# Kernel optimization log

Measured on AMD Instinct MI355X. Metric: run time of the kernel, lower is better.

Reference implementation:

```python
import jax, jax.numpy as jnp
import numpy as np

THRESHOLD = 0.5
NEG_POS_RATIO = 3
ALPHA = 1.0
B, P, C, O = 128, 8732, 21, 32


def xy_to_cxcy(xy):
    return jnp.concatenate([(xy[..., 2:] + xy[..., :2]) / 2, xy[..., 2:] - xy[..., :2]], axis=-1)


def cxcy_to_xy(cxcy):
    return jnp.concatenate([cxcy[..., :2] - cxcy[..., 2:] / 2, cxcy[..., :2] + cxcy[..., 2:] / 2], axis=-1)


def cxcy_to_gcxgcy(cxcy, priors_cxcy):
    g_cxcy = (cxcy[..., :2] - priors_cxcy[..., :2]) / (priors_cxcy[..., 2:] / 10.0)
    g_wh = jnp.log(cxcy[..., 2:] / priors_cxcy[..., 2:]) * 5.0
    return jnp.concatenate([g_cxcy, g_wh], axis=-1)


def find_jaccard_overlap(set1, set2):
    # set1: [O,4] xy, set2: [P,4] xy -> [O,P]
    lo = jnp.maximum(set1[:, None, :2], set2[None, :, :2])
    hi = jnp.minimum(set1[:, None, 2:], set2[None, :, 2:])
    inter = jnp.prod(jnp.clip(hi - lo, 0.0), axis=-1)
    a1 = jnp.prod(set1[:, 2:] - set1[:, :2], axis=-1)
    a2 = jnp.prod(set2[:, 2:] - set2[:, :2], axis=-1)
    union = a1[:, None] + a2[None, :] - inter
    return inter / union


def setup_inputs() -> dict:
    key = jax.random.key(0)
    k0, k1, k2, k3, k4, k5, k6 = jax.random.split(key, 7)
    predicted_locs = jax.random.normal(k0, (B, P, 4), jnp.float32)
    predicted_scores = jax.random.normal(k1, (B, P, C), jnp.float32)
    centers = jax.random.uniform(k2, (B, O, 2), jnp.float32, 0.2, 0.8)
    sizes = jax.random.uniform(k3, (B, O, 2), jnp.float32, 0.05, 0.3)
    boxes = jnp.concatenate([centers - sizes / 2, centers + sizes / 2], axis=-1)
    labels = jax.random.randint(k4, (B, O), 0, C)
    p_c = jax.random.uniform(k5, (P, 2), jnp.float32, 0.05, 0.95)
    p_wh = jax.random.uniform(k6, (P, 2), jnp.float32, 0.05, 0.5)
    priors_cxcy = jnp.concatenate([p_c, p_wh], axis=-1)
    return {"predicted_locs": predicted_locs, "predicted_scores": predicted_scores,
            "boxes": boxes, "labels": labels, "priors_cxcy": priors_cxcy}


def reference(predicted_locs, predicted_scores, boxes, labels, priors_cxcy):
    priors_xy = cxcy_to_xy(priors_cxcy)

    def match_one(boxes_i, labels_i):
        overlap = find_jaccard_overlap(boxes_i, priors_xy)           # [O,P]
        overlap_for_each_prior = jnp.max(overlap, axis=0)            # [P]
        object_for_each_prior = jnp.argmax(overlap, axis=0)          # [P]
        prior_for_each_object = jnp.argmax(overlap, axis=1)          # [O]
        object_for_each_prior = object_for_each_prior.at[prior_for_each_object].set(jnp.arange(O))
        overlap_for_each_prior = overlap_for_each_prior.at[prior_for_each_object].set(1.0)
        label_for_each_prior = labels_i[object_for_each_prior]
        label_for_each_prior = jnp.where(overlap_for_each_prior < THRESHOLD, 0, label_for_each_prior)
        true_locs_i = cxcy_to_gcxgcy(xy_to_cxcy(boxes_i[object_for_each_prior]), priors_cxcy)
        return label_for_each_prior, true_locs_i

    true_classes, true_locs = jax.vmap(match_one)(boxes, labels)     # [B,P], [B,P,4]

    positive = true_classes != 0                                     # [B,P]
    n_positives = jnp.sum(positive, axis=1)                          # [B]
    n_pos_total = jnp.sum(n_positives)

    # L1Loss (mean over selected positive elements, 4 per prior)
    abs_diff = jnp.abs(predicted_locs - true_locs)                   # [B,P,4]
    loc_loss = jnp.sum(abs_diff * positive[..., None]) / (n_pos_total.astype(jnp.float32) * 4.0)

    # per-element cross-entropy
    log_p = jax.nn.log_softmax(predicted_scores, axis=-1)            # [B,P,C]
    conf_loss_all = -jnp.take_along_axis(log_p, true_classes[..., None], axis=-1)[..., 0]  # [B,P]

    conf_loss_pos_sum = jnp.sum(jnp.where(positive, conf_loss_all, 0.0))
    conf_loss_neg = jnp.where(positive, 0.0, conf_loss_all)
    conf_loss_neg_sorted = -jnp.sort(-conf_loss_neg, axis=1)         # descending
    n_hard = NEG_POS_RATIO * n_positives                             # [B]
    hard_mask = jnp.arange(P)[None, :] < n_hard[:, None]             # [B,P]
    conf_loss_hard_neg_sum = jnp.sum(jnp.where(hard_mask, conf_loss_neg_sorted, 0.0))

    conf_loss = (conf_loss_hard_neg_sum + conf_loss_pos_sum) / n_pos_total.astype(jnp.float32)
    return conf_loss + ALPHA * loc_loss
```

## Files before the change

### kernel.cpp

```cpp
#include <hip/hip_runtime.h>
#include <hip/hip_bf16.h>

#define NB 128
#define NP 8732
#define NO 32
#define NC 21


__global__ __launch_bounds__(256) void k_init(int* ws) {
    int i = blockIdx.x * 256 + threadIdx.x;
    const int n = 36352 / 4;
    if (i < n) ws[i] = 0;
}

__global__ __launch_bounds__(256) void k_match(const float* __restrict__ boxes,
                                               const float* __restrict__ priors,
                                               int* __restrict__ code,
                                               unsigned long long* __restrict__ packed) {
    int b = blockIdx.y;
    int base = blockIdx.x * 1024 + threadIdx.x;
    int lane = threadIdx.x & 63;

    __shared__ float4 sbox[NO];
    if (threadIdx.x < NO)
        sbox[threadIdx.x] = ((const float4*)(boxes + (size_t)b * NO * 4))[threadIdx.x];
    __syncthreads();

    int   pidx[4];
    float px1[4], py1[4], px2[4], py2[4], pa[4];
    float bestv[4];
    int   besto[4];
#pragma unroll
    for (int j = 0; j < 4; ++j) {
        int p = base + 256 * j;
        pidx[j] = p;
        int pp = p < NP ? p : NP - 1;
        float4 pr = ((const float4*)priors)[pp];
        px1[j] = pr.x - pr.z * 0.5f; py1[j] = pr.y - pr.w * 0.5f;
        px2[j] = pr.x + pr.z * 0.5f; py2[j] = pr.y + pr.w * 0.5f;
        pa[j]  = (px2[j] - px1[j]) * (py2[j] - py1[j]);
        bestv[j] = -1.0f; besto[j] = 0;
    }

    for (int o = 0; o < NO; ++o) {
        float4 bx = sbox[o];
        float a1 = (bx.z - bx.x) * (bx.w - bx.y);
        unsigned long long pk = 0ull;
#pragma unroll
        for (int j = 0; j < 4; ++j) {
            float lx = fmaxf(bx.x, px1[j]), ly = fmaxf(bx.y, py1[j]);
            float hx = fminf(bx.z, px2[j]), hy = fminf(bx.w, py2[j]);
            float iw = fmaxf(hx - lx, 0.0f), ih = fmaxf(hy - ly, 0.0f);
            float inter = iw * ih;
            float iou = inter / (a1 + pa[j] - inter);
            if (iou > bestv[j]) { bestv[j] = iou; besto[j] = o; }
            if (pidx[j] < NP) {
                unsigned long long key =
                    ((unsigned long long)__float_as_uint(iou) << 32) |
                    (unsigned long long)(0xFFFFFFFFu - (unsigned)pidx[j]);
                if (key > pk) pk = key;
            }
        }
        for (int s = 32; s > 0; s >>= 1) {
            unsigned long long other = __shfl_xor(pk, s, 64);
            if (other > pk) pk = other;
        }
        if (lane == 0) atomicMax(&packed[b * NO + o], pk);
    }
#pragma unroll
    for (int j = 0; j < 4; ++j)
        if (pidx[j] < NP)
            code[(size_t)b * NP + pidx[j]] = besto[j] | (bestv[j] >= 0.5f ? 256 : 0);
}

__global__ void k_force(int* __restrict__ code,
                        const unsigned long long* __restrict__ packed) {
    int b = threadIdx.x;
    if (b >= NB) return;
    for (int o = 0; o < NO; ++o) {
        unsigned long long pk = packed[b * NO + o];
        unsigned p = 0xFFFFFFFFu - (unsigned)(pk & 0xFFFFFFFFull);
        if (p < NP) code[(size_t)b * NP + p] = o | 256;
    }
}

__global__ __launch_bounds__(256) void k_loss(const float* __restrict__ plocs,
                                              const float* __restrict__ scores,
                                              const float* __restrict__ boxes,
                                              const int* __restrict__ labels,
                                              const float* __restrict__ priors,
                                              const int* __restrict__ code,
                                              float* __restrict__ confneg,
                                              int* __restrict__ npos,
                                              double* __restrict__ accb) {
    __shared__ float srow[256 * NC];
    int b = blockIdx.y;
    int p0 = blockIdx.x * 256;
    int cnt = NP - p0; if (cnt > 256) cnt = 256;
    int nf4 = cnt * NC / 4;
    const float4* src4 = (const float4*)(scores + ((size_t)b * NP + p0) * NC);
    for (int i = threadIdx.x; i < nf4; i += 256)
        ((float4*)srow)[i] = src4[i];
    __syncthreads();

    int p = p0 + threadIdx.x;
    float posconf = 0.0f, locpart = 0.0f;
    int isp = 0;

    if (p < NP) {
        int cd = code[(size_t)b * NP + p];
        int obj = cd & 255;
        int lbl = (cd & 256) ? labels[b * NO + obj] : 0;

        const float* s = srow + threadIdx.x * NC;
        float m = s[0];
#pragma unroll
        for (int c = 1; c < NC; ++c) m = fmaxf(m, s[c]);
        float sum = 0.0f;
#pragma unroll
        for (int c = 0; c < NC; ++c) sum += __expf(s[c] - m);
        float conf = m + __logf(sum) - s[lbl];

        if (lbl != 0) {
            isp = 1;
            posconf = conf;
            float4 bx = ((const float4*)boxes)[b * NO + obj];
            float4 pr = ((const float4*)priors)[p];
            float cx = (bx.x + bx.z) * 0.5f, cy = (bx.y + bx.w) * 0.5f;
            float w = bx.z - bx.x, h = bx.w - bx.y;
            float gx = (cx - pr.x) / (pr.z * 0.1f);
            float gy = (cy - pr.y) / (pr.w * 0.1f);
            float gw = __logf(w / pr.z) * 5.0f;
            float gh = __logf(h / pr.w) * 5.0f;
            float4 pl = ((const float4*)plocs)[(size_t)b * NP + p];
            locpart = fabsf(pl.x - gx) + fabsf(pl.y - gy) +
                      fabsf(pl.z - gw) + fabsf(pl.w - gh);
        }
        confneg[(size_t)b * NP + p] = isp ? 0.0f : conf;
    }

    for (int s = 32; s > 0; s >>= 1) {
        posconf += __shfl_xor(posconf, s, 64);
        locpart += __shfl_xor(locpart, s, 64);
        isp     += __shfl_xor(isp, s, 64);
    }
    __shared__ float w0[4], w1[4];
    __shared__ int wc[4];
    int wid = threadIdx.x >> 6, lane = threadIdx.x & 63;
    if (lane == 0) { w0[wid] = posconf; w1[wid] = locpart; wc[wid] = isp; }
    __syncthreads();
    if (threadIdx.x == 0) {
        float t0 = w0[0] + w0[1] + w0[2] + w0[3];
        float t1 = w1[0] + w1[1] + w1[2] + w1[3];
        int   tc = wc[0] + wc[1] + wc[2] + wc[3];
        atomicAdd(&npos[b], tc);
        atomicAdd(&accb[b * 3 + 0], (double)t0);
        atomicAdd(&accb[b * 3 + 1], (double)t1);
    }
}

__global__ __launch_bounds__(1024) void k_topk(const float* __restrict__ confneg,
                                               const int* __restrict__ npos,
                                               double* __restrict__ accb) {
    __shared__ int   si[16];
    __shared__ double sd[16];
    __shared__ int   sbcast;
    int tid = threadIdx.x, b = blockIdx.x;
    int lane = tid & 63, wid = tid >> 6;

    const float* src = confneg + (size_t)b * NP;
    float val[9];
#pragma unroll
    for (int j = 0; j < 9; ++j) {
        int i = tid + j * 1024;
        val[j] = (i < NP) ? src[i] : 0.0f;
    }
    int k = npos[b] * 3;
    if (k > NP) k = NP;
    if (k <= 0) return;

    unsigned T = 0;
    for (int bit = 30; bit >= 0; --bit) {
        unsigned cand = T | (1u << bit);
        int cnt = 0;
#pragma unroll
        for (int j = 0; j < 9; ++j)
            cnt += (__float_as_uint(val[j]) >= cand) ? 1 : 0;
        for (int s = 32; s > 0; s >>= 1) cnt += __shfl_xor(cnt, s, 64);
        if (lane == 0) si[wid] = cnt;
        __syncthreads();
        if (tid == 0) {
            int t = 0;
            for (int w = 0; w < 16; ++w) t += si[w];
            sbcast = t;
        }
        __syncthreads();
        if (sbcast >= k) T = cand;
    }

    int cgt = 0;
    double sgt = 0.0;
#pragma unroll
    for (int j = 0; j < 9; ++j) {
        unsigned u = __float_as_uint(val[j]);
        if (u > T) { cgt++; sgt += (double)val[j]; }
    }
    for (int s = 32; s > 0; s >>= 1) {
        cgt += __shfl_xor(cgt, s, 64);
        sgt += __shfl_xor(sgt, s, 64);
    }
    if (lane == 0) { si[wid] = cgt; sd[wid] = sgt; }
    __syncthreads();
    if (tid == 0) {
        int cg = 0; double sg = 0.0;
        for (int w = 0; w < 16; ++w) { cg += si[w]; sg += sd[w]; }
        accb[b * 3 + 2] = sg + (double)(k - cg) * (double)__uint_as_float(T);
    }
}

__global__ __launch_bounds__(128) void k_final(const int* __restrict__ npos,
                                               const double* __restrict__ accb,
                                               float* __restrict__ out) {
    int b = threadIdx.x;
    double pc = accb[b * 3 + 0];
    double lc = accb[b * 3 + 1];
    double hn = accb[b * 3 + 2];
    double np_ = (double)npos[b];
    for (int s = 32; s > 0; s >>= 1) {
        pc  += __shfl_xor(pc, s, 64);
        lc  += __shfl_xor(lc, s, 64);
        hn  += __shfl_xor(hn, s, 64);
        np_ += __shfl_xor(np_, s, 64);
    }
    __shared__ double sD[4][2];
    int wid = threadIdx.x >> 6, lane = threadIdx.x & 63;
    if (lane == 0) { sD[0][wid] = pc; sD[1][wid] = lc; sD[2][wid] = hn; sD[3][wid] = np_; }
    __syncthreads();
    if (threadIdx.x == 0) {
        double P = sD[0][0] + sD[0][1];
        double L = sD[1][0] + sD[1][1];
        double H = sD[2][0] + sD[2][1];
        double nt = sD[3][0] + sD[3][1];
        out[0] = (float)((H + P) / nt + L / (nt * 4.0));
    }
}

extern "C" void kernel_launch(void* const* d_in, const int* in_sizes, int n_in,
                              void* d_out, int out_size, void* d_ws, size_t ws_size,
                              hipStream_t stream) {
    const float* plocs  = (const float*)d_in[0];
    const float* scores = (const float*)d_in[1];
    const float* boxes  = (const float*)d_in[2];
    const int*   labels = (const int*)d_in[3];
    const float* priors = (const float*)d_in[4];
    float* out = (float*)d_out;

    char* ws = (char*)d_ws;
    unsigned long long* packed = (unsigned long long*)ws;
    int*    npos    = (int*)(ws + 32768);
    double* accb    = (double*)(ws + 33280);
    int*    code    = (int*)(ws + 36352);
    float*  confneg = (float*)(ws + 36352 + (size_t)NB * NP * 4);

    hipLaunchKernelGGL(k_init, dim3((36352 / 4 + 255) / 256), dim3(256), 0, stream, (int*)ws);
    hipLaunchKernelGGL(k_match, dim3((NP + 1023) / 1024, NB), dim3(256), 0, stream,
                       boxes, priors, code, packed);
    hipLaunchKernelGGL(k_force, dim3(1), dim3(128), 0, stream, code, packed);
    hipLaunchKernelGGL(k_loss, dim3((NP + 255) / 256, NB), dim3(256), 0, stream,
                       plocs, scores, boxes, labels, priors, code, confneg, npos, accb);
    hipLaunchKernelGGL(k_topk, dim3(NB), dim3(1024), 0, stream, confneg, npos, accb);
    hipLaunchKernelGGL(k_final, dim3(1), dim3(128), 0, stream, npos, accb, out);
}
```

Measured before the change: 248.7 us.

## Split prior matching into per-prior and per-object kernels

Splits the matching kernel in two. The per-prior kernel keeps only best-object tracking. A new per-object kernel stages a chunk of priors in shared memory and has each wave reduce argmax over priors for 8 objects, which replaces the 32 per-block shuffle reductions and atomics in the original. IoU is now computed twice and one extra kernel launch is added. k_force also preloads all packed values into registers before scattering.

```diff
diff --git a/kernel.cpp b/kernel.cpp
--- a/kernel.cpp
+++ b/kernel.cpp
@@ -5,6 +5,7 @@
 #define NP 8732
 #define NO 32
 #define NC 21
+#define PCHUNK 2183
 
 
 __global__ __launch_bounds__(256) void k_init(int* ws) {
@@ -13,13 +14,11 @@
     if (i < n) ws[i] = 0;
 }
 
-__global__ __launch_bounds__(256) void k_match(const float* __restrict__ boxes,
-                                               const float* __restrict__ priors,
-                                               int* __restrict__ code,
-                                               unsigned long long* __restrict__ packed) {
+__global__ __launch_bounds__(256) void k_match_prior(const float* __restrict__ boxes,
+                                                     const float* __restrict__ priors,
+                                                     int* __restrict__ code) {
     int b = blockIdx.y;
     int base = blockIdx.x * 1024 + threadIdx.x;
-    int lane = threadIdx.x & 63;
 
     __shared__ float4 sbox[NO];
     if (threadIdx.x < NO)
@@ -45,7 +44,6 @@
     for (int o = 0; o < NO; ++o) {
         float4 bx = sbox[o];
         float a1 = (bx.z - bx.x) * (bx.w - bx.y);
-        unsigned long long pk = 0ull;
 #pragma unroll
         for (int j = 0; j < 4; ++j) {
             float lx = fmaxf(bx.x, px1[j]), ly = fmaxf(bx.y, py1[j]);
@@ -54,32 +52,68 @@
             float inter = iw * ih;
             float iou = inter / (a1 + pa[j] - inter);
             if (iou > bestv[j]) { bestv[j] = iou; besto[j] = o; }
-            if (pidx[j] < NP) {
-                unsigned long long key =
-                    ((unsigned long long)__float_as_uint(iou) << 32) |
-                    (unsigned long long)(0xFFFFFFFFu - (unsigned)pidx[j]);
-                if (key > pk) pk = key;
-            }
-        }
-        for (int s = 32; s > 0; s >>= 1) {
-            unsigned long long other = __shfl_xor(pk, s, 64);
-            if (other > pk) pk = other;
-        }
-        if (lane == 0) atomicMax(&packed[b * NO + o], pk);
+        }
     }
 #pragma unroll
     for (int j = 0; j < 4; ++j)
         if (pidx[j] < NP)
             code[(size_t)b * NP + pidx[j]] = besto[j] | (bestv[j] >= 0.5f ? 256 : 0);
+}
+
+__global__ __launch_bounds__(256) void k_match_obj(const float* __restrict__ boxes,
+                                                   const float* __restrict__ priors,
+                                                   unsigned long long* __restrict__ packed) {
+    __shared__ float4 spri[PCHUNK];
+    int b = blockIdx.y;
+    int pbeg = blockIdx.x * PCHUNK;
+    int n = NP - pbeg; if (n > PCHUNK) n = PCHUNK;
+
+    for (int i = threadIdx.x; i < n; i += 256) {
+        float4 pr = ((const float4*)priors)[pbeg + i];
+        float x1 = pr.x - pr.z * 0.5f, y1 = pr.y - pr.w * 0.5f;
+        float x2 = pr.x + pr.z * 0.5f, y2 = pr.y + pr.w * 0.5f;
+        spri[i] = make_float4(x1, y1, x2, y2);
+    }
+    __syncthreads();
+
+    int wid = threadIdx.x >> 6, lane = threadIdx.x & 63;
+#pragma unroll
+    for (int oo = 0; oo < 8; ++oo) {
+        int o = wid * 8 + oo;
+        float4 bx = ((const float4*)boxes)[b * NO + o];
+        float a1 = (bx.z - bx.x) * (bx.w - bx.y);
+        unsigned long long pk = 0ull;
+        for (int i = lane; i < n; i += 64) {
+            float4 pr = spri[i];
+            float lx = fmaxf(bx.x, pr.x), ly = fmaxf(bx.y, pr.y);
+            float hx = fminf(bx.z, pr.z), hy = fminf(bx.w, pr.w);
+            float iw = fmaxf(hx - lx, 0.0f), ih = fmaxf(hy - ly, 0.0f);
+            float inter = iw * ih;
+            float pa = (pr.z - pr.x) * (pr.w - pr.y);
+            float iou = inter / (a1 + pa - inter);
+            unsigned long long key =
+                ((unsigned long long)__float_as_uint(iou) << 32) |
+                (unsigned long long)(0xFFFFFFFFu - (unsigned)(pbeg + i));
+            if (key > pk) pk = key;
+        }
+        for (int s = 32; s > 0; s >>= 1) {
+            unsigned long long t = __shfl_xor(pk, s, 64);
+            if (t > pk) pk = t;
+        }
+        if (lane == 0) atomicMax(&packed[b * NO + o], pk);
+    }
 }
 
 __global__ void k_force(int* __restrict__ code,
                         const unsigned long long* __restrict__ packed) {
     int b = threadIdx.x;
     if (b >= NB) return;
+    unsigned long long pk[NO];
+#pragma unroll
+    for (int o = 0; o < NO; ++o) pk[o] = packed[b * NO + o];
+#pragma unroll
     for (int o = 0; o < NO; ++o) {
-        unsigned long long pk = packed[b * NO + o];
-        unsigned p = 0xFFFFFFFFu - (unsigned)(pk & 0xFFFFFFFFull);
+        unsigned p = 0xFFFFFFFFu - (unsigned)(pk[o] & 0xFFFFFFFFull);
         if (p < NP) code[(size_t)b * NP + p] = o | 256;
     }
 }
@@ -263,8 +297,10 @@
     float*  confneg = (float*)(ws + 36352 + (size_t)NB * NP * 4);
 
     hipLaunchKernelGGL(k_init, dim3((36352 / 4 + 255) / 256), dim3(256), 0, stream, (int*)ws);
-    hipLaunchKernelGGL(k_match, dim3((NP + 1023) / 1024, NB), dim3(256), 0, stream,
-                       boxes, priors, code, packed);
+    hipLaunchKernelGGL(k_match_prior, dim3((NP + 1023) / 1024, NB), dim3(256), 0, stream,
+                       boxes, priors, code);
+    hipLaunchKernelGGL(k_match_obj, dim3(4, NB), dim3(256), 0, stream,
+                       boxes, priors, packed);
     hipLaunchKernelGGL(k_force, dim3(1), dim3(128), 0, stream, code, packed);
     hipLaunchKernelGGL(k_loss, dim3((NP + 255) / 256, NB), dim3(256), 0, stream,
                        plocs, scores, boxes, labels, priors, code, confneg, npos, accb);
```

New measurement: 269.0 us. +8.2%, slower.

## Fuse all loss stages into one cooperative persistent kernel with grid syncs

Applied to the files above, without the earlier changes.

Replaces six separate kernel launches (init, match, force, loss, top-k, final) with a single cooperative kernel of 512 blocks that uses grid-wide syncs between phases. Each block handles a quarter of one image's priors, staging priors in shared memory during matching. The top-k phase now runs on 256 threads with 35 values each instead of 1024 threads with 9. This removes launch gaps and inter-kernel overhead, at the cost of grid.sync barriers and reduced parallelism in the serial phases (top-k, force), and it depends on all 512 blocks being co-resident.

```diff
diff --git a/kernel.cpp b/kernel.cpp
--- a/kernel.cpp
+++ b/kernel.cpp
@@ -1,247 +1,242 @@
 #include <hip/hip_runtime.h>
-#include <hip/hip_bf16.h>
+#include <hip/hip_cooperative_groups.h>
+
+namespace cg = cooperative_groups;
 
 #define NB 128
 #define NP 8732
 #define NO 32
 #define NC 21
-
-
-__global__ __launch_bounds__(256) void k_init(int* ws) {
-    int i = blockIdx.x * 256 + threadIdx.x;
-    const int n = 36352 / 4;
-    if (i < n) ws[i] = 0;
-}
-
-__global__ __launch_bounds__(256) void k_match(const float* __restrict__ boxes,
-                                               const float* __restrict__ priors,
-                                               int* __restrict__ code,
-                                               unsigned long long* __restrict__ packed) {
-    int b = blockIdx.y;
-    int base = blockIdx.x * 1024 + threadIdx.x;
-    int lane = threadIdx.x & 63;
-
-    __shared__ float4 sbox[NO];
-    if (threadIdx.x < NO)
-        sbox[threadIdx.x] = ((const float4*)(boxes + (size_t)b * NO * 4))[threadIdx.x];
-    __syncthreads();
-
-    int   pidx[4];
-    float px1[4], py1[4], px2[4], py2[4], pa[4];
-    float bestv[4];
-    int   besto[4];
-#pragma unroll
-    for (int j = 0; j < 4; ++j) {
-        int p = base + 256 * j;
-        pidx[j] = p;
-        int pp = p < NP ? p : NP - 1;
-        float4 pr = ((const float4*)priors)[pp];
-        px1[j] = pr.x - pr.z * 0.5f; py1[j] = pr.y - pr.w * 0.5f;
-        px2[j] = pr.x + pr.z * 0.5f; py2[j] = pr.y + pr.w * 0.5f;
-        pa[j]  = (px2[j] - px1[j]) * (py2[j] - py1[j]);
-        bestv[j] = -1.0f; besto[j] = 0;
-    }
-
-    for (int o = 0; o < NO; ++o) {
-        float4 bx = sbox[o];
-        float a1 = (bx.z - bx.x) * (bx.w - bx.y);
-        unsigned long long pk = 0ull;
-#pragma unroll
-        for (int j = 0; j < 4; ++j) {
-            float lx = fmaxf(bx.x, px1[j]), ly = fmaxf(bx.y, py1[j]);
-            float hx = fminf(bx.z, px2[j]), hy = fminf(bx.w, py2[j]);
-            float iw = fmaxf(hx - lx, 0.0f), ih = fmaxf(hy - ly, 0.0f);
-            float inter = iw * ih;
-            float iou = inter / (a1 + pa[j] - inter);
-            if (iou > bestv[j]) { bestv[j] = iou; besto[j] = o; }
-            if (pidx[j] < NP) {
-                unsigned long long key =
-                    ((unsigned long long)__float_as_uint(iou) << 32) |
-                    (unsigned long long)(0xFFFFFFFFu - (unsigned)pidx[j]);
-                if (key > pk) pk = key;
+#define NCH 4
+#define CPB 2304
+#define NBLK (NB * NCH)
+
+
+__global__ __launch_bounds__(256, 2) void k_fused(
+    const float* __restrict__ plocs, const float* __restrict__ scores,
+    const float* __restrict__ boxes, const int* __restrict__ labels,
+    const float* __restrict__ priors,
+    unsigned long long* packed, int* npos, double* accb,
+    int* code, float* confneg, float* out, int* zbase) {
+    cg::grid_group grid = cg::this_grid();
+    const int bid = blockIdx.x, tid = threadIdx.x;
+    const int lane = tid & 63, wid = tid >> 6;
+
+    __shared__ union {
+        struct { float4 box[NO]; float4 pri[CPB]; } a;
+        float srow[256 * NC];
+    } sm;
+    __shared__ float sw0[4], sw1[4];
+    __shared__ int swc[4], sig[4], ssum;
+    __shared__ double sdg[4];
+    __shared__ unsigned long long sforce[NO];
+    __shared__ double sfin[4][4];
+
+    const int b = bid >> 2;
+    const int c = bid & 3;
+    const int pbeg = c * CPB;
+    const int n = min(CPB, NP - pbeg);
+
+    { int i = bid * 256 + tid; if (i < 36352 / 4) zbase[i] = 0; }
+    grid.sync();
+
+    {
+        if (tid < NO) sm.a.box[tid] = ((const float4*)boxes)[b * NO + tid];
+        for (int i = tid; i < n; i += 256) {
+            float4 pr = ((const float4*)priors)[pbeg + i];
+            sm.a.pri[i] = make_float4(pr.x - pr.z * 0.5f, pr.y - pr.w * 0.5f,
+                                      pr.x + pr.z * 0.5f, pr.y + pr.w * 0.5f);
+        }
+        __syncthreads();
+
+        float x1[9], y1[9], x2[9], y2[9], ar[9], bv[9];
+        int bo[9];
+#pragma unroll
+        for (int j = 0; j < 9; ++j) {
+            int i = tid + j * 256;
+            int ic = i < n ? i : 0;
+            float4 pr = sm.a.pri[ic];
+            x1[j] = pr.x; y1[j] = pr.y; x2[j] = pr.z; y2[j] = pr.w;
+            ar[j] = (pr.z - pr.x) * (pr.w - pr.y);
+            bv[j] = -1.0f; bo[j] = 0;
+        }
+
+        for (int o = 0; o < NO; ++o) {
+            float4 bx = sm.a.box[o];
+            float a1 = (bx.z - bx.x) * (bx.w - bx.y);
+            unsigned long long pk = 0ull;
+#pragma unroll
+            for (int j = 0; j < 9; ++j) {
+                int i = tid + j * 256;
+                float lx = fmaxf(bx.x, x1[j]), ly = fmaxf(bx.y, y1[j]);
+                float hx = fminf(bx.z, x2[j]), hy = fminf(bx.w, y2[j]);
+                float iw = fmaxf(hx - lx, 0.0f), ih = fmaxf(hy - ly, 0.0f);
+                float inter = iw * ih;
+                float iou = inter / (a1 + ar[j] - inter);
+                if (i < n) {
+                    if (iou > bv[j]) { bv[j] = iou; bo[j] = o; }
+                    unsigned long long key =
+                        ((unsigned long long)__float_as_uint(iou) << 32) |
+                        (unsigned long long)(0xFFFFFFFFu - (unsigned)(pbeg + i));
+                    if (key > pk) pk = key;
+                }
+            }
+            for (int s = 32; s > 0; s >>= 1) {
+                unsigned long long t = __shfl_xor(pk, s, 64);
+                if (t > pk) pk = t;
+            }
+            if (lane == 0) atomicMax(&packed[b * NO + o], pk);
+        }
+#pragma unroll
+        for (int j = 0; j < 9; ++j) {
+            int i = tid + j * 256;
+            if (i < n)
+                code[(size_t)b * NP + pbeg + i] = bo[j] | (bv[j] >= 0.5f ? 256 : 0);
+        }
+    }
+    grid.sync();
+
+    if (bid < NB) {
+        if (tid < NO) sforce[tid] = packed[bid * NO + tid];
+        __syncthreads();
+        if (tid == 0) {
+#pragma unroll
+            for (int o = 0; o < NO; ++o) {
+                unsigned p = 0xFFFFFFFFu - (unsigned)(sforce[o] & 0xFFFFFFFFull);
+                code[(size_t)bid * NP + p] = o | 256;
+            }
+        }
+    }
+    grid.sync();
+
+    {
+        float posconf = 0.0f, locpart = 0.0f;
+        int isp = 0;
+        for (int t0 = 0; t0 < n; t0 += 256) {
+            int cnt = min(256, n - t0);
+            int nf4 = cnt * NC / 4;
+            const float4* src4 = (const float4*)(scores + ((size_t)b * NP + pbeg + t0) * NC);
+            __syncthreads();
+            for (int i = tid; i < nf4; i += 256) ((float4*)sm.srow)[i] = src4[i];
+            __syncthreads();
+            if (tid < cnt) {
+                int p = pbeg + t0 + tid;
+                int cd = code[(size_t)b * NP + p];
+                int obj = cd & 255;
+                int lbl = (cd & 256) ? labels[b * NO + obj] : 0;
+                const float* s = sm.srow + tid * NC;
+                float m = s[0];
+#pragma unroll
+                for (int cc = 1; cc < NC; ++cc) m = fmaxf(m, s[cc]);
+                float sum = 0.0f;
+#pragma unroll
+                for (int cc = 0; cc < NC; ++cc) sum += __expf(s[cc] - m);
+                float conf = m + __logf(sum) - s[lbl];
+                if (lbl != 0) {
+                    isp++;
+                    posconf += conf;
+                    float4 bx = ((const float4*)boxes)[b * NO + obj];
+                    float4 pr = ((const float4*)priors)[p];
+                    float cx = (bx.x + bx.z) * 0.5f, cy = (bx.y + bx.w) * 0.5f;
+                    float w = bx.z - bx.x, h = bx.w - bx.y;
+                    float gx = (cx - pr.x) / (pr.z * 0.1f);
+                    float gy = (cy - pr.y) / (pr.w * 0.1f);
+                    float gw = __logf(w / pr.z) * 5.0f;
+                    float gh = __logf(h / pr.w) * 5.0f;
+                    float4 pl = ((const float4*)plocs)[(size_t)b * NP + p];
+                    locpart += fabsf(pl.x - gx) + fabsf(pl.y - gy) +
+                               fabsf(pl.z - gw) + fabsf(pl.w - gh);
+                    confneg[(size_t)b * NP + p] = 0.0f;
+                } else {
+                    confneg[(size_t)b * NP + p] = conf;
+                }
             }
         }
         for (int s = 32; s > 0; s >>= 1) {
-            unsigned long long other = __shfl_xor(pk, s, 64);
-            if (other > pk) pk = other;
-        }
-        if (lane == 0) atomicMax(&packed[b * NO + o], pk);
-    }
-#pragma unroll
-    for (int j = 0; j < 4; ++j)
-        if (pidx[j] < NP)
-            code[(size_t)b * NP + pidx[j]] = besto[j] | (bestv[j] >= 0.5f ? 256 : 0);
-}
-
-__global__ void k_force(int* __restrict__ code,
-                        const unsigned long long* __restrict__ packed) {
-    int b = threadIdx.x;
-    if (b >= NB) return;
-    for (int o = 0; o < NO; ++o) {
-        unsigned long long pk = packed[b * NO + o];
-        unsigned p = 0xFFFFFFFFu - (unsigned)(pk & 0xFFFFFFFFull);
-        if (p < NP) code[(size_t)b * NP + p] = o | 256;
-    }
-}
-
-__global__ __launch_bounds__(256) void k_loss(const float* __restrict__ plocs,
-                                              const float* __restrict__ scores,
-                                              const float* __restrict__ boxes,
-                                              const int* __restrict__ labels,
-                                              const float* __restrict__ priors,
-                                              const int* __restrict__ code,
-                                              float* __restrict__ confneg,
-                                              int* __restrict__ npos,
-                                              double* __restrict__ accb) {
-    __shared__ float srow[256 * NC];
-    int b = blockIdx.y;
-    int p0 = blockIdx.x * 256;
-    int cnt = NP - p0; if (cnt > 256) cnt = 256;
-    int nf4 = cnt * NC / 4;
-    const float4* src4 = (const float4*)(scores + ((size_t)b * NP + p0) * NC);
-    for (int i = threadIdx.x; i < nf4; i += 256)
-        ((float4*)srow)[i] = src4[i];
-    __syncthreads();
-
-    int p = p0 + threadIdx.x;
-    float posconf = 0.0f, locpart = 0.0f;
-    int isp = 0;
-
-    if (p < NP) {
-        int cd = code[(size_t)b * NP + p];
-        int obj = cd & 255;
-        int lbl = (cd & 256) ? labels[b * NO + obj] : 0;
-
-        const float* s = srow + threadIdx.x * NC;
-        float m = s[0];
-#pragma unroll
-        for (int c = 1; c < NC; ++c) m = fmaxf(m, s[c]);
-        float sum = 0.0f;
-#pragma unroll
-        for (int c = 0; c < NC; ++c) sum += __expf(s[c] - m);
-        float conf = m + __logf(sum) - s[lbl];
-
-        if (lbl != 0) {
-            isp = 1;
-            posconf = conf;
-            float4 bx = ((const float4*)boxes)[b * NO + obj];
-            float4 pr = ((const float4*)priors)[p];
-            float cx = (bx.x + bx.z) * 0.5f, cy = (bx.y + bx.w) * 0.5f;
-            float w = bx.z - bx.x, h = bx.w - bx.y;
-            float gx = (cx - pr.x) / (pr.z * 0.1f);
-            float gy = (cy - pr.y) / (pr.w * 0.1f);
-            float gw = __logf(w / pr.z) * 5.0f;
-            float gh = __logf(h / pr.w) * 5.0f;
-            float4 pl = ((const float4*)plocs)[(size_t)b * NP + p];
-            locpart = fabsf(pl.x - gx) + fabsf(pl.y - gy) +
-                      fabsf(pl.z - gw) + fabsf(pl.w - gh);
-        }
-        confneg[(size_t)b * NP + p] = isp ? 0.0f : conf;
-    }
-
-    for (int s = 32; s > 0; s >>= 1) {
-        posconf += __shfl_xor(posconf, s, 64);
-        locpart += __shfl_xor(locpart, s, 64);
-        isp     += __shfl_xor(isp, s, 64);
-    }
-    __shared__ float w0[4], w1[4];
-    __shared__ int wc[4];
-    int wid = threadIdx.x >> 6, lane = threadIdx.x & 63;
-    if (lane == 0) { w0[wid] = posconf; w1[wid] = locpart; wc[wid] = isp; }
-    __syncthreads();
-    if (threadIdx.x == 0) {
-        float t0 = w0[0] + w0[1] + w0[2] + w0[3];
-        float t1 = w1[0] + w1[1] + w1[2] + w1[3];
-        int   tc = wc[0] + wc[1] + wc[2] + wc[3];
-        atomicAdd(&npos[b], tc);
-        atomicAdd(&accb[b * 3 + 0], (double)t0);
-        atomicAdd(&accb[b * 3 + 1], (double)t1);
-    }
-}
-
-__global__ __launch_bounds__(1024) void k_topk(const float* __restrict__ confneg,
-                                               const int* __restrict__ npos,
-                                               double* __restrict__ accb) {
-    __shared__ int   si[16];
-    __shared__ double sd[16];
-    __shared__ int   sbcast;
-    int tid = threadIdx.x, b = blockIdx.x;
-    int lane = tid & 63, wid = tid >> 6;
-
-    const float* src = confneg + (size_t)b * NP;
-    float val[9];
-#pragma unroll
-    for (int j = 0; j < 9; ++j) {
-        int i = tid + j * 1024;
-        val[j] = (i < NP) ? src[i] : 0.0f;
-    }
-    int k = npos[b] * 3;
-    if (k > NP) k = NP;
-    if (k <= 0) return;
-
-    unsigned T = 0;
-    for (int bit = 30; bit >= 0; --bit) {
-        unsigned cand = T | (1u << bit);
-        int cnt = 0;
-#pragma unroll
-        for (int j = 0; j < 9; ++j)
-            cnt += (__float_as_uint(val[j]) >= cand) ? 1 : 0;
-        for (int s = 32; s > 0; s >>= 1) cnt += __shfl_xor(cnt, s, 64);
-        if (lane == 0) si[wid] = cnt;
+            posconf += __shfl_xor(posconf, s, 64);
+            locpart += __shfl_xor(locpart, s, 64);
+            isp     += __shfl_xor(isp, s, 64);
+        }
+        if (lane == 0) { sw0[wid] = posconf; sw1[wid] = locpart; swc[wid] = isp; }
         __syncthreads();
         if (tid == 0) {
-            int t = 0;
-            for (int w = 0; w < 16; ++w) t += si[w];
-            sbcast = t;
-        }
-        __syncthreads();
-        if (sbcast >= k) T = cand;
-    }
-
-    int cgt = 0;
-    double sgt = 0.0;
-#pragma unroll
-    for (int j = 0; j < 9; ++j) {
-        unsigned u = __float_as_uint(val[j]);
-        if (u > T) { cgt++; sgt += (double)val[j]; }
-    }
-    for (int s = 32; s > 0; s >>= 1) {
-        cgt += __shfl_xor(cgt, s, 64);
-        sgt += __shfl_xor(sgt, s, 64);
-    }
-    if (lane == 0) { si[wid] = cgt; sd[wid] = sgt; }
-    __syncthreads();
-    if (tid == 0) {
-        int cg = 0; double sg = 0.0;
-        for (int w = 0; w < 16; ++w) { cg += si[w]; sg += sd[w]; }
-        accb[b * 3 + 2] = sg + (double)(k - cg) * (double)__uint_as_float(T);
-    }
-}
-
-__global__ __launch_bounds__(128) void k_final(const int* __restrict__ npos,
-                                               const double* __restrict__ accb,
-                                               float* __restrict__ out) {
-    int b = threadIdx.x;
-    double pc = accb[b * 3 + 0];
-    double lc = accb[b * 3 + 1];
-    double hn = accb[b * 3 + 2];
-    double np_ = (double)npos[b];
-    for (int s = 32; s > 0; s >>= 1) {
-        pc  += __shfl_xor(pc, s, 64);
-        lc  += __shfl_xor(lc, s, 64);
-        hn  += __shfl_xor(hn, s, 64);
-        np_ += __shfl_xor(np_, s, 64);
-    }
-    __shared__ double sD[4][2];
-    int wid = threadIdx.x >> 6, lane = threadIdx.x & 63;
-    if (lane == 0) { sD[0][wid] = pc; sD[1][wid] = lc; sD[2][wid] = hn; sD[3][wid] = np_; }
-    __syncthreads();
-    if (threadIdx.x == 0) {
-        double P = sD[0][0] + sD[0][1];
-        double L = sD[1][0] + sD[1][1];
-        double H = sD[2][0] + sD[2][1];
-        double nt = sD[3][0] + sD[3][1];
-        out[0] = (float)((H + P) / nt + L / (nt * 4.0));
+            atomicAdd(&npos[b], swc[0] + swc[1] + swc[2] + swc[3]);
+            atomicAdd(&accb[b * 3 + 0], (double)(sw0[0] + sw0[1] + sw0[2] + sw0[3]));
+            atomicAdd(&accb[b * 3 + 1], (double)(sw1[0] + sw1[1] + sw1[2] + sw1[3]));
+        }
+    }
+    grid.sync();
+
+    if (bid < NB) {
+        const float* src = confneg + (size_t)bid * NP;
+        float val[35];
+#pragma unroll
+        for (int j = 0; j < 35; ++j) {
+            int i = tid + j * 256;
+            val[j] = (i < NP) ? src[i] : 0.0f;
+        }
+        int k = npos[bid] * 3;
+        if (k > NP) k = NP;
+        if (k > 0) {
+            unsigned T = 0;
+            for (int bit = 30; bit >= 0; --bit) {
+                unsigned cand = T | (1u << bit);
+                int cnt = 0;
+#pragma unroll
+                for (int j = 0; j < 35; ++j)
+                    cnt += (__float_as_uint(val[j]) >= cand) ? 1 : 0;
+                for (int s = 32; s > 0; s >>= 1) cnt += __shfl_xor(cnt, s, 64);
+                if (lane == 0) sig[wid] = cnt;
+                __syncthreads();
+                if (tid == 0) ssum = sig[0] + sig[1] + sig[2] + sig[3];
+                __syncthreads();
+                if (ssum >= k) T = cand;
+            }
+            int cgt = 0;
+            double sgt = 0.0;
+#pragma unroll
+            for (int j = 0; j < 35; ++j) {
+                unsigned u = __float_as_uint(val[j]);
+                if (u > T) { cgt++; sgt += (double)val[j]; }
+            }
+            for (int s = 32; s > 0; s >>= 1) {
+                cgt += __shfl_xor(cgt, s, 64);
+                sgt += __shfl_xor(sgt, s, 64);
+            }
+            if (lane == 0) { sig[wid] = cgt; sdg[wid] = sgt; }
+            __syncthreads();
+            if (tid == 0) {
+                int cg = sig[0] + sig[1] + sig[2] + sig[3];
+                double sg = sdg[0] + sdg[1] + sdg[2] + sdg[3];
+                accb[bid * 3 + 2] = sg + (double)(k - cg) * (double)__uint_as_float(T);
+            }
+        }
+    }
+    grid.sync();
+
+    if (bid == 0) {
+        double pc = 0, lc = 0, hn = 0, nn = 0;
+        if (tid < NB) {
+            pc = accb[tid * 3 + 0];
+            lc = accb[tid * 3 + 1];
+            hn = accb[tid * 3 + 2];
+            nn = (double)npos[tid];
+        }
+        for (int s = 32; s > 0; s >>= 1) {
+            pc += __shfl_xor(pc, s, 64);
+            lc += __shfl_xor(lc, s, 64);
+            hn += __shfl_xor(hn, s, 64);
+            nn += __shfl_xor(nn, s, 64);
+        }
+        if (lane == 0) { sfin[0][wid] = pc; sfin[1][wid] = lc; sfin[2][wid] = hn; sfin[3][wid] = nn; }
+        __syncthreads();
+        if (tid == 0) {
+            double P  = sfin[0][0] + sfin[0][1] + sfin[0][2] + sfin[0][3];
+            double L  = sfin[1][0] + sfin[1][1] + sfin[1][2] + sfin[1][3];
+            double H  = sfin[2][0] + sfin[2][1] + sfin[2][2] + sfin[2][3];
+            double NT = sfin[3][0] + sfin[3][1] + sfin[3][2] + sfin[3][3];
+            out[0] = (float)((H + P) / NT + L / (NT * 4.0));
+        }
     }
 }
 
@@ -261,13 +256,13 @@
     double* accb    = (double*)(ws + 33280);
     int*    code    = (int*)(ws + 36352);
     float*  confneg = (float*)(ws + 36352 + (size_t)NB * NP * 4);
-
-    hipLaunchKernelGGL(k_init, dim3((36352 / 4 + 255) / 256), dim3(256), 0, stream, (int*)ws);
-    hipLaunchKernelGGL(k_match, dim3((NP + 1023) / 1024, NB), dim3(256), 0, stream,
-                       boxes, priors, code, packed);
-    hipLaunchKernelGGL(k_force, dim3(1), dim3(128), 0, stream, code, packed);
-    hipLaunchKernelGGL(k_loss, dim3((NP + 255) / 256, NB), dim3(256), 0, stream,
-                       plocs, scores, boxes, labels, priors, code, confneg, npos, accb);
-    hipLaunchKernelGGL(k_topk, dim3(NB), dim3(1024), 0, stream, confneg, npos, accb);
-    hipLaunchKernelGGL(k_final, dim3(1), dim3(128), 0, stream, npos, accb, out);
+    int*    zbase   = (int*)ws;
+
+    void* args[] = {
+        (void*)&plocs, (void*)&scores, (void*)&boxes, (void*)&labels, (void*)&priors,
+        (void*)&packed, (void*)&npos, (void*)&accb, (void*)&code, (void*)&confneg,
+        (void*)&out, (void*)&zbase
+    };
+    hipLaunchCooperativeKernel((const void*)k_fused, dim3(NBLK), dim3(256),
+                               args, 0, stream);
 }
```

Measured after the change: 519.7 us. 109% more time.
